# Kernel tuning notes

Measured on AMD Instinct MI355X. Metric: run time of the kernel, lower is better.

## Reference

```python
import jax, jax.numpy as jnp
import numpy as np

D_MODEL = 1024
HEADS = 16
DK = D_MODEL // HEADS
B, S = 2, 2048


def setup_inputs() -> dict:
    key = jax.random.key(0)
    ks = jax.random.split(key, 9)
    s = 0.02
    return {
        "Q": jax.random.normal(ks[0], (B, S, D_MODEL), jnp.float32),
        "K": jax.random.normal(ks[1], (B, S, D_MODEL), jnp.float32),
        "V": jax.random.normal(ks[2], (B, S, D_MODEL), jnp.float32),
        "mask": jnp.ones((B, 1, S), jnp.int32),
        "Wq": jax.random.normal(ks[3], (D_MODEL, D_MODEL), jnp.float32) * s,
        "Wk": jax.random.normal(ks[4], (D_MODEL, D_MODEL), jnp.float32) * s,
        "Wv": jax.random.normal(ks[5], (D_MODEL, D_MODEL), jnp.float32) * s,
        "Wo": jax.random.normal(ks[6], (D_MODEL, D_MODEL), jnp.float32) * s,
        "ln_gamma": jnp.ones((D_MODEL,), jnp.float32),
        "ln_beta": jnp.zeros((D_MODEL,), jnp.float32),
    }


def _layer_norm(x, gamma, beta, eps=1e-5):
    mu = jnp.mean(x, axis=-1, keepdims=True)
    var = jnp.mean(jnp.square(x - mu), axis=-1, keepdims=True)
    return (x - mu) * jax.lax.rsqrt(var + eps) * gamma + beta


def reference(Q, K, V, mask, Wq, Wk, Wv, Wo, ln_gamma, ln_beta):
    # torch Linear(no bias): y = x @ W.T
    def split_heads(x):  # [B,S,D] -> [B,H,S,dk]
        return x.reshape(B, -1, HEADS, DK).transpose(0, 2, 1, 3)

    q = split_heads(Q @ Wq.T)
    k = split_heads(K @ Wk.T)
    v = split_heads(V @ Wv.T)

    # scores: [B,H,Sq,Sk]
    scores = jnp.einsum("bhqd,bhkd->bhqk", q, k) / np.sqrt(DK).astype(np.float32)
    m = mask[:, None, :, :]  # [B,1,1,S] broadcast over heads and queries
    scores = jnp.where(m == 0, -jnp.inf, scores)
    attn = jax.nn.softmax(scores, axis=-1)  # dropout is identity in eval
    out = jnp.einsum("bhqk,bhkd->bhqd", attn, v)
    out = out.transpose(0, 2, 1, 3).reshape(B, -1, D_MODEL)
    out = out @ Wo.T
    return _layer_norm(out + Q, ln_gamma, ln_beta)
```

## Files before the change

kernel.cpp:

```cpp
#include <hip/hip_runtime.h>
#include <hip/hip_bf16.h>
#include <stdint.h>

#define NB 2
#define NS 2048
#define ND 1024
#define NH 16
#define NDK 64
#define NM (NB*NS)

using bf16x8 = __attribute__((ext_vector_type(8))) short;
using f32x4  = __attribute__((ext_vector_type(4))) float;
using f32x16 = __attribute__((ext_vector_type(16))) float;
using u32x4  = __attribute__((ext_vector_type(4))) unsigned;

__device__ __forceinline__ unsigned short f2bf(float f){
  unsigned u = __float_as_uint(f);
  u += 0x7fffu + ((u>>16)&1u);
  return (unsigned short)(u>>16);
}

__device__ __forceinline__ void gload_lds16(const void* g, void* l){
  __builtin_amdgcn_global_load_lds((const __attribute__((address_space(1))) void*)g,
                                   (__attribute__((address_space(3))) void*)l, 16, 0, 0);
}

__device__ __forceinline__ float fexp2(float x){
#if __has_builtin(__builtin_amdgcn_exp2f)
  return __builtin_amdgcn_exp2f(x);
#else
  return __expf(x * 0.69314718056f);
#endif
}

__device__ __forceinline__ unsigned cvtpk_bf16(float lo, float hi){
  unsigned r;
  asm("v_cvt_pk_bf16_f32 %0, %1, %2" : "=v"(r) : "v"(lo), "v"(hi));
  return r;
}

__device__ __forceinline__ void swap32(unsigned &a, unsigned &b){
#if __has_builtin(__builtin_amdgcn_permlane32_swap)
  auto rr = __builtin_amdgcn_permlane32_swap((int)a, (int)b, false, false);
  a = (unsigned)rr[0]; b = (unsigned)rr[1];
#else
  const bool lo = (threadIdx.x & 32) == 0;
  unsigned sa = (unsigned)__shfl_xor((int)a, 32, 64);
  unsigned sb = (unsigned)__shfl_xor((int)b, 32, 64);
  unsigned na = lo ? a : sb;
  unsigned nb = lo ? sa : b;
  a = na; b = nb;
#endif
}

__device__ __forceinline__ f32x16 mfma32(bf16x8 a, bf16x8 b, f32x16 c){
  return __builtin_amdgcn_mfma_f32_32x32x16_bf16(a, b, c, 0, 0, 0);
}

__global__ __launch_bounds__(256) void prep_k(const float* __restrict__ Q, const float* __restrict__ K,
                                              const float* __restrict__ V, const float* __restrict__ Wq,
                                              const float* __restrict__ Wk, const float* __restrict__ Wv,
                                              const float* __restrict__ Wo,
                                              unsigned short* __restrict__ Xbf,
                                              unsigned short* __restrict__ Wbf){
  const int bid = blockIdx.x;
  const float* src; unsigned short* dst; int i;
  if (bid < 12288){
    const int which = bid >> 12;
    src = (which==0) ? Q : (which==1) ? K : V;
    dst = Xbf + ((size_t)which << 22);
    i = (bid & 4095)*256 + threadIdx.x;
  } else {
    const int which = (bid - 12288) >> 10;
    src = (which==0) ? Wq : (which==1) ? Wk : (which==2) ? Wv : Wo;
    dst = Wbf + ((size_t)which << 20);
    i = ((bid - 12288) & 1023)*256 + threadIdx.x;
  }
  float4 v = ((const float4*)src)[i];
  ushort4 o;
  o.x = f2bf(v.x); o.y = f2bf(v.y); o.z = f2bf(v.z); o.w = f2bf(v.w);
  ((ushort4*)dst)[i] = o;
}

__device__ void gemm128_core(const short* __restrict__ A, const short* __restrict__ W,
                             void* __restrict__ out, int mode){
  __shared__ short lsA[2][4096];
  __shared__ short lsB[2][4096];
  const int tid = threadIdx.x;
  const int m0 = blockIdx.y*128, n0 = blockIdx.x*128;
  const short* gA = A + (size_t)m0*1024;
  const short* gB = W + (size_t)n0*1024;
  const int srow = tid>>2, scol = (tid&3)*8;
  const int w = tid>>6, lane = tid&63, lr = lane&15, lk = lane>>4;
  const int wm = w>>1, wn = w&1;

  f32x4 acc[4][4];
  #pragma unroll
  for (int i=0;i<4;++i)
    #pragma unroll
    for (int j=0;j<4;++j) acc[i][j] = (f32x4){0.f,0.f,0.f,0.f};

  #pragma unroll
  for (int r=0;r<2;++r){
    gload_lds16(gA + (size_t)(r*64+srow)*1024 + scol, &lsA[0][(r*256+tid)*8]);
    gload_lds16(gB + (size_t)(r*64+srow)*1024 + scol, &lsB[0][(r*256+tid)*8]);
  }
  int cur = 0;
  for (int ks=0; ks<32; ++ks){
    __syncthreads();
    if (ks+1 < 32){
      const int k0 = (ks+1)*32;
      #pragma unroll
      for (int r=0;r<2;++r){
        gload_lds16(gA + (size_t)(r*64+srow)*1024 + k0 + scol, &lsA[cur^1][(r*256+tid)*8]);
        gload_lds16(gB + (size_t)(r*64+srow)*1024 + k0 + scol, &lsB[cur^1][(r*256+tid)*8]);
      }
    }
    bf16x8 af[4], bfr[4];
    #pragma unroll
    for (int i=0;i<4;++i){
      af[i]  = *(const bf16x8*)&lsA[cur][(wm*64+i*16+lr)*32 + lk*8];
      bfr[i] = *(const bf16x8*)&lsB[cur][(wn*64+i*16+lr)*32 + lk*8];
    }
    #pragma unroll
    for (int i=0;i<4;++i)
      #pragma unroll
      for (int j=0;j<4;++j)
        acc[i][j] = __builtin_amdgcn_mfma_f32_16x16x32_bf16(af[i], bfr[j], acc[i][j], 0,0,0);
    cur ^= 1;
  }
  #pragma unroll
  for (int i=0;i<4;++i)
    #pragma unroll
    for (int j=0;j<4;++j)
      #pragma unroll
      for (int r=0;r<4;++r){
        const int m = m0 + wm*64 + i*16 + lk*4 + r;
        const int n = n0 + wn*64 + j*16 + lr;
        const float v = acc[i][j][r];
        if (mode == 2){
          ((float*)out)[(size_t)m*1024 + n] = v;
        } else {
          const int b = m>>11, s = m&2047, h = n>>6, dk = n&63;
          size_t addr;
          if (mode == 0) addr = (((size_t)(b*NH+h))*NS + s)*NDK + dk;
          else           addr = (((size_t)(b*NH+h))*NDK + dk)*NS + s;
          ((unsigned short*)out)[addr] = f2bf(v);
        }
      }
}

__global__ __launch_bounds__(256) void gemm_qkv(const short* __restrict__ Xbf, const short* __restrict__ Wbf,
                                                unsigned short* qh, unsigned short* kh, unsigned short* vT){
  const int z = blockIdx.z;
  const short* A = Xbf + (size_t)z*NM*ND;
  const short* W = Wbf + (size_t)z*ND*ND;
  void* out = (z==0) ? (void*)qh : (z==1) ? (void*)kh : (void*)vT;
  gemm128_core(A, W, out, (z==2) ? 1 : 0);
}

__global__ __launch_bounds__(256) void gemm_out(const short* __restrict__ Attn, const short* __restrict__ Wo,
                                                float* proj){
  gemm128_core(Attn, Wo, proj, 2);
}

__global__ __launch_bounds__(512) void attn_k(const short* __restrict__ qh, const short* __restrict__ kh,
                                              const short* __restrict__ vT, const int* __restrict__ mask,
                                              unsigned short* __restrict__ attn){
  __shared__ char sb[32768];
  const int bid = blockIdx.x;
  const int qb = bid & 7, h = (bid>>3)&15, b = bid>>7;
  const int tid = threadIdx.x, w = tid>>6, lane = tid&63;
  const int ql = lane & 31, hi = lane>>5;
  const int bh = b*NH + h;
  const int q0 = qb*256 + w*32;
  const float C2 = 0.18033688f;

  const int D = tid*16;
  const int strow = D>>7;
  const int S = D ^ ((strow&7)<<4);
  const char* ksrc  = (const char*)(kh + (size_t)bh*NS*NDK) + S;
  const char* vsrc  = (const char*)(vT + ((size_t)bh*NDK + strow)*NS) + (S & 127);

  const short* qrow = qh + ((size_t)bh*NS + q0 + ql)*NDK + hi*8;
  bf16x8 qf[4];
  #pragma unroll
  for (int kp=0;kp<4;++kp) qf[kp] = *(const bf16x8*)(qrow + kp*16);

  const int* mrow = mask + b*NS;

  f32x16 o0, o1;
  #pragma unroll
  for (int r=0;r<16;++r){ o0[r]=0.f; o1[r]=0.f; }
  float mrun = -1e30f, lrun = 0.f;

  const int swz = (ql&7)<<4;

  gload_lds16(ksrc, sb + D);
  gload_lds16(vsrc, sb + 16384 + D);

  for (int kt=0; kt<32; ++kt){
    const int kv0 = kt*64;
    const int buf = (kt&1)*8192;
    __syncthreads();
    if (kt+1 < 32){
      const int nbuf = ((kt+1)&1)*8192;
      gload_lds16(ksrc + (size_t)(kv0+64)*128, sb + nbuf + D);
      gload_lds16(vsrc + (size_t)(kv0+64)*2,   sb + 16384 + nbuf + D);
    }
    const unsigned long long bal = __ballot(mrow[kv0 + lane] != 0);
    const unsigned mw0 = (unsigned)bal, mw1 = (unsigned)(bal>>32);
    const bool allm = (~bal) == 0ull;

    bf16x8 kf[8];
    #pragma unroll
    for (int kvh=0;kvh<2;++kvh)
      #pragma unroll
      for (int kp=0;kp<4;++kp)
        kf[kvh*4+kp] = *(const bf16x8*)(sb + buf + (((kvh*32+ql)*128 + kp*32 + hi*16) ^ swz));

    f32x16 s0, s1;
    #pragma unroll
    for (int r=0;r<16;++r){ s0[r]=0.f; s1[r]=0.f; }
    #pragma unroll
    for (int kp=0;kp<4;++kp){
      s0 = mfma32(kf[kp],   qf[kp], s0);
      s1 = mfma32(kf[4+kp], qf[kp], s1);
    }

    float t[16];
    #pragma unroll
    for (int r=0;r<16;++r) t[r] = fmaxf(s0[r], s1[r]);
    #pragma unroll
    for (int st=8; st>=1; st>>=1)
      #pragma unroll
      for (int r=0;r<st;++r) t[r] = fmaxf(t[r], t[r+st]);
    const float tm = fmaxf(t[0], __shfl_xor(t[0], 32, 64));

    if (!__all(tm - mrun <= 32.f)){
      const float mnew = fmaxf(mrun, tm);
      const float fac  = fexp2((mrun - mnew)*C2);
      mrun = mnew;
      #pragma unroll
      for (int r=0;r<16;++r){ o0[r]*=fac; o1[r]*=fac; }
      lrun *= fac;
    }
    const float nb = mrun*C2;

    bf16x8 vf[8];
    #pragma unroll
    for (int dh=0;dh<2;++dh)
      #pragma unroll
      for (int c=0;c<4;++c)
        vf[dh*4+c] = *(const bf16x8*)(sb + 16384 + buf + (((dh*32+ql)*128 + c*32 + hi*16) ^ swz));

    float psum = 0.f;
    #pragma unroll
    for (int kvh=0; kvh<2; ++kvh){
      const f32x16& ss = kvh ? s1 : s0;
      const unsigned mw = kvh ? mw1 : mw0;
      unsigned pwd[8];
      float ps0 = 0.f, ps1 = 0.f;
      #pragma unroll
      for (int i=0;i<8;++i){
        const int bp0 = ((2*i)&3) + 8*((2*i)>>2);
        float p0 = fexp2(ss[2*i]*C2   - nb);
        float p1 = fexp2(ss[2*i+1]*C2 - nb);
        if (!allm){
          p0 = ((mw >> (bp0     + 4*hi)) & 1u) ? p0 : 0.f;
          p1 = ((mw >> (bp0 + 1 + 4*hi)) & 1u) ? p1 : 0.f;
        }
        ps0 += p0; ps1 += p1;
        pwd[i] = cvtpk_bf16(p0, p1);
      }
      psum += ps0 + ps1;
      swap32(pwd[0], pwd[2]);
      swap32(pwd[1], pwd[3]);
      swap32(pwd[4], pwd[6]);
      swap32(pwd[5], pwd[7]);
      u32x4 c0w = {pwd[0], pwd[1], pwd[2], pwd[3]};
      u32x4 c1w = {pwd[4], pwd[5], pwd[6], pwd[7]};
      bf16x8 pf0 = __builtin_bit_cast(bf16x8, c0w);
      bf16x8 pf1 = __builtin_bit_cast(bf16x8, c1w);
      o0 = mfma32(vf[0*4 + 2*kvh],     pf0, o0);
      o1 = mfma32(vf[1*4 + 2*kvh],     pf0, o1);
      o0 = mfma32(vf[0*4 + 2*kvh + 1], pf1, o0);
      o1 = mfma32(vf[1*4 + 2*kvh + 1], pf1, o1);
    }
    psum += __shfl_xor(psum, 32, 64);
    lrun += psum;
  }

  __syncthreads();
  const float inv = 1.f / lrun;
  char* ep = sb + w*4096;
  #pragma unroll
  for (int dh=0; dh<2; ++dh){
    const f32x16& oo = dh ? o1 : o0;
    #pragma unroll
    for (int i=0;i<8;++i){
      const int d0 = ((2*i)&3) + 8*((2*i)>>2) + 4*hi + dh*32;
      const unsigned pk = cvtpk_bf16(oo[2*i]*inv, oo[2*i+1]*inv);
      *(unsigned*)(ep + (((ql*128) + d0*2) ^ ((ql&7)<<4))) = pk;
    }
  }
  asm volatile("s_waitcnt lgkmcnt(0)" ::: "memory");
  #pragma unroll
  for (int seg=0; seg<4; ++seg){
    const int qq = seg*8 + (lane>>3), dc = (lane&7)*8;
    bf16x8 vv = *(const bf16x8*)(ep + (((qq*128) + dc*2) ^ ((qq&7)<<4)));
    *(bf16x8*)(attn + ((size_t)b*NS + q0 + qq)*ND + h*NDK + dc) = vv;
  }
}

__global__ __launch_bounds__(256) void ln_k(const float* __restrict__ proj, const float* __restrict__ Qin,
                                            const float* __restrict__ gamma, const float* __restrict__ beta,
                                            float* __restrict__ out){
  const int row = blockIdx.x*4 + (threadIdx.x>>6);
  const int lane = threadIdx.x & 63;
  const float4* pp = (const float4*)(proj + (size_t)row*ND);
  const float4* qq = (const float4*)(Qin + (size_t)row*ND);
  float4 x[4];
  float sum = 0.f;
  #pragma unroll
  for (int i=0;i<4;++i){
    const float4 a = pp[lane + i*64];
    const float4 bq = qq[lane + i*64];
    x[i].x = a.x+bq.x; x[i].y = a.y+bq.y; x[i].z = a.z+bq.z; x[i].w = a.w+bq.w;
    sum += x[i].x + x[i].y + x[i].z + x[i].w;
  }
  #pragma unroll
  for (int off=32; off>=1; off>>=1) sum += __shfl_xor(sum, off, 64);
  const float mu = sum * (1.f/1024.f);
  float vs = 0.f;
  #pragma unroll
  for (int i=0;i<4;++i){
    float d0=x[i].x-mu, d1=x[i].y-mu, d2=x[i].z-mu, d3=x[i].w-mu;
    vs += d0*d0 + d1*d1 + d2*d2 + d3*d3;
  }
  #pragma unroll
  for (int off=32; off>=1; off>>=1) vs += __shfl_xor(vs, off, 64);
  const float rstd = rsqrtf(vs*(1.f/1024.f) + 1e-5f);
  #pragma unroll
  for (int i=0;i<4;++i){
    const float4 g  = ((const float4*)gamma)[lane + i*64];
    const float4 be = ((const float4*)beta)[lane + i*64];
    float4 y;
    y.x = (x[i].x-mu)*rstd*g.x + be.x;
    y.y = (x[i].y-mu)*rstd*g.y + be.y;
    y.z = (x[i].z-mu)*rstd*g.z + be.z;
    y.w = (x[i].w-mu)*rstd*g.w + be.w;
    ((float4*)(out + (size_t)row*ND))[lane + i*64] = y;
  }
}

extern "C" void kernel_launch(void* const* d_in, const int* in_sizes, int n_in,
                              void* d_out, int out_size, void* d_ws, size_t ws_size,
                              hipStream_t stream){
  const float* Q    = (const float*)d_in[0];
  const float* K    = (const float*)d_in[1];
  const float* V    = (const float*)d_in[2];
  const int*   mask = (const int*)  d_in[3];
  const float* Wq   = (const float*)d_in[4];
  const float* Wk   = (const float*)d_in[5];
  const float* Wv   = (const float*)d_in[6];
  const float* Wo   = (const float*)d_in[7];
  const float* gam  = (const float*)d_in[8];
  const float* bet  = (const float*)d_in[9];
  float* out = (float*)d_out;
  char* ws = (char*)d_ws;

  unsigned short* Wbf  = (unsigned short*)(ws);
  unsigned short* Xbf  = (unsigned short*)(ws + (size_t)(8u<<20));
  unsigned short* qhp  = (unsigned short*)(ws + (size_t)(32u<<20));
  unsigned short* khp  = (unsigned short*)(ws + (size_t)(40u<<20));
  unsigned short* vTp  = (unsigned short*)(ws + (size_t)(48u<<20));
  unsigned short* attb = (unsigned short*)(ws + (size_t)(56u<<20));
  float* proj  = (float*)(ws + (size_t)(8u<<20));

  prep_k<<<16384,256,0,stream>>>(Q, K, V, Wq, Wk, Wv, Wo, Xbf, Wbf);

  gemm_qkv<<<dim3(8,32,3),256,0,stream>>>((const short*)Xbf, (const short*)Wbf, qhp, khp, vTp);

  attn_k<<<256,512,0,stream>>>((const short*)qhp, (const short*)khp, (const short*)vTp, mask, attb);

  gemm_out<<<dim3(8,32),256,0,stream>>>((const short*)attb, (const short*)(Wbf + (3u<<20)), proj);

  ln_k<<<1024,256,0,stream>>>(proj, Q, gam, bet, out);
}
```

Baseline: 171.6 us.

## Use 256x128 QKV GEMM tiles, XCD-aware block remap, fuse residual into out-proj

The QKV projection GEMM now computes a 256x128 tile per block, with two A sub-tiles sharing each B fragment, which halves the number of B loads per output. Launches are flattened to 1D and blocks are remapped so neighbouring logical tiles land on the same XCD, which should improve L2 reuse. The residual add of Q moves into the output-projection GEMM epilogue, so the layer-norm kernel no longer reads Q. The trade-off is more accumulator registers (32 f32x4 per thread) and only 384 blocks in the QKV GEMM, which may lower occupancy.

```diff
diff --git a/kernel.cpp b/kernel.cpp
--- a/kernel.cpp
+++ b/kernel.cpp
@@ -82,28 +82,40 @@
   ((ushort4*)dst)[i] = o;
 }
 
-__device__ void gemm128_core(const short* __restrict__ A, const short* __restrict__ W,
-                             void* __restrict__ out, int mode){
-  __shared__ short lsA[2][4096];
+__global__ __launch_bounds__(256) void gemm_qkv(const short* __restrict__ Xbf, const short* __restrict__ Wbf,
+                                                unsigned short* __restrict__ qh, unsigned short* __restrict__ kh,
+                                                unsigned short* __restrict__ vT){
+  __shared__ short lsA[2][2][4096];
   __shared__ short lsB[2][4096];
   const int tid = threadIdx.x;
-  const int m0 = blockIdx.y*128, n0 = blockIdx.x*128;
-  const short* gA = A + (size_t)m0*1024;
-  const short* gB = W + (size_t)n0*1024;
+  const int hw = blockIdx.x;
+  const int logical = (hw & 7)*48 + (hw >> 3);
+  const int z = logical >> 7, rem = logical & 127;
+  const int my = rem >> 3, nx = rem & 7;
+  const short* A = Xbf + (size_t)z*NM*ND;
+  const short* W = Wbf + (size_t)z*ND*ND;
+  unsigned short* out = (z==0) ? qh : (z==1) ? kh : vT;
+  const int mode = (z==2) ? 1 : 0;
+  const int m0 = my*256, n0 = nx*128;
+
+  const short* gA0 = A + (size_t)m0*1024;
+  const short* gA1 = A + (size_t)(m0+128)*1024;
+  const short* gB  = W + (size_t)n0*1024;
   const int srow = tid>>2, scol = (tid&3)*8;
   const int w = tid>>6, lane = tid&63, lr = lane&15, lk = lane>>4;
   const int wm = w>>1, wn = w&1;
 
-  f32x4 acc[4][4];
+  f32x4 acc0[4][4], acc1[4][4];
   #pragma unroll
   for (int i=0;i<4;++i)
     #pragma unroll
-    for (int j=0;j<4;++j) acc[i][j] = (f32x4){0.f,0.f,0.f,0.f};
+    for (int j=0;j<4;++j){ acc0[i][j] = (f32x4){0.f,0.f,0.f,0.f}; acc1[i][j] = (f32x4){0.f,0.f,0.f,0.f}; }
 
   #pragma unroll
   for (int r=0;r<2;++r){
-    gload_lds16(gA + (size_t)(r*64+srow)*1024 + scol, &lsA[0][(r*256+tid)*8]);
-    gload_lds16(gB + (size_t)(r*64+srow)*1024 + scol, &lsB[0][(r*256+tid)*8]);
+    gload_lds16(gA0 + (size_t)(r*64+srow)*1024 + scol, &lsA[0][0][(r*256+tid)*8]);
+    gload_lds16(gA1 + (size_t)(r*64+srow)*1024 + scol, &lsA[0][1][(r*256+tid)*8]);
+    gload_lds16(gB  + (size_t)(r*64+srow)*1024 + scol, &lsB[0][(r*256+tid)*8]);
   }
   int cur = 0;
   for (int ks=0; ks<32; ++ks){
@@ -112,56 +124,111 @@
       const int k0 = (ks+1)*32;
       #pragma unroll
       for (int r=0;r<2;++r){
-        gload_lds16(gA + (size_t)(r*64+srow)*1024 + k0 + scol, &lsA[cur^1][(r*256+tid)*8]);
-        gload_lds16(gB + (size_t)(r*64+srow)*1024 + k0 + scol, &lsB[cur^1][(r*256+tid)*8]);
+        gload_lds16(gA0 + (size_t)(r*64+srow)*1024 + k0 + scol, &lsA[cur^1][0][(r*256+tid)*8]);
+        gload_lds16(gA1 + (size_t)(r*64+srow)*1024 + k0 + scol, &lsA[cur^1][1][(r*256+tid)*8]);
+        gload_lds16(gB  + (size_t)(r*64+srow)*1024 + k0 + scol, &lsB[cur^1][(r*256+tid)*8]);
       }
     }
-    bf16x8 af[4], bfr[4];
-    #pragma unroll
-    for (int i=0;i<4;++i){
-      af[i]  = *(const bf16x8*)&lsA[cur][(wm*64+i*16+lr)*32 + lk*8];
-      bfr[i] = *(const bf16x8*)&lsB[cur][(wn*64+i*16+lr)*32 + lk*8];
-    }
+    bf16x8 bfr[4], af[4];
+    #pragma unroll
+    for (int j=0;j<4;++j) bfr[j] = *(const bf16x8*)&lsB[cur][(wn*64+j*16+lr)*32 + lk*8];
+    #pragma unroll
+    for (int i=0;i<4;++i) af[i] = *(const bf16x8*)&lsA[cur][0][(wm*64+i*16+lr)*32 + lk*8];
     #pragma unroll
     for (int i=0;i<4;++i)
       #pragma unroll
       for (int j=0;j<4;++j)
-        acc[i][j] = __builtin_amdgcn_mfma_f32_16x16x32_bf16(af[i], bfr[j], acc[i][j], 0,0,0);
+        acc0[i][j] = __builtin_amdgcn_mfma_f32_16x16x32_bf16(af[i], bfr[j], acc0[i][j], 0,0,0);
+    #pragma unroll
+    for (int i=0;i<4;++i) af[i] = *(const bf16x8*)&lsA[cur][1][(wm*64+i*16+lr)*32 + lk*8];
+    #pragma unroll
+    for (int i=0;i<4;++i)
+      #pragma unroll
+      for (int j=0;j<4;++j)
+        acc1[i][j] = __builtin_amdgcn_mfma_f32_16x16x32_bf16(af[i], bfr[j], acc1[i][j], 0,0,0);
     cur ^= 1;
   }
   #pragma unroll
-  for (int i=0;i<4;++i)
-    #pragma unroll
-    for (int j=0;j<4;++j)
-      #pragma unroll
-      for (int r=0;r<4;++r){
-        const int m = m0 + wm*64 + i*16 + lk*4 + r;
-        const int n = n0 + wn*64 + j*16 + lr;
-        const float v = acc[i][j][r];
-        if (mode == 2){
-          ((float*)out)[(size_t)m*1024 + n] = v;
-        } else {
+  for (int sub=0; sub<2; ++sub){
+    const int mb = m0 + sub*128;
+    #pragma unroll
+    for (int i=0;i<4;++i)
+      #pragma unroll
+      for (int j=0;j<4;++j)
+        #pragma unroll
+        for (int r=0;r<4;++r){
+          const int m = mb + wm*64 + i*16 + lk*4 + r;
+          const int n = n0 + wn*64 + j*16 + lr;
+          const float v = sub ? acc1[i][j][r] : acc0[i][j][r];
           const int b = m>>11, s = m&2047, h = n>>6, dk = n&63;
           size_t addr;
           if (mode == 0) addr = (((size_t)(b*NH+h))*NS + s)*NDK + dk;
           else           addr = (((size_t)(b*NH+h))*NDK + dk)*NS + s;
-          ((unsigned short*)out)[addr] = f2bf(v);
+          out[addr] = f2bf(v);
         }
+  }
+}
+
+__global__ __launch_bounds__(256) void gemm_out(const short* __restrict__ Attn, const short* __restrict__ Wo,
+                                                const float* __restrict__ Qin, float* __restrict__ proj){
+  __shared__ short lsA[2][4096];
+  __shared__ short lsB[2][4096];
+  const int tid = threadIdx.x;
+  const int hw = blockIdx.x;
+  const int logical = (hw & 7)*32 + (hw >> 3);
+  const int my = logical >> 3, nx = logical & 7;
+  const int m0 = my*128, n0 = nx*128;
+  const short* gA = Attn + (size_t)m0*1024;
+  const short* gB = Wo + (size_t)n0*1024;
+  const int srow = tid>>2, scol = (tid&3)*8;
+  const int w = tid>>6, lane = tid&63, lr = lane&15, lk = lane>>4;
+  const int wm = w>>1, wn = w&1;
+
+  f32x4 acc[4][4];
+  #pragma unroll
+  for (int i=0;i<4;++i)
+    #pragma unroll
+    for (int j=0;j<4;++j) acc[i][j] = (f32x4){0.f,0.f,0.f,0.f};
+
+  #pragma unroll
+  for (int r=0;r<2;++r){
+    gload_lds16(gA + (size_t)(r*64+srow)*1024 + scol, &lsA[0][(r*256+tid)*8]);
+    gload_lds16(gB + (size_t)(r*64+srow)*1024 + scol, &lsB[0][(r*256+tid)*8]);
+  }
+  int cur = 0;
+  for (int ks=0; ks<32; ++ks){
+    __syncthreads();
+    if (ks+1 < 32){
+      const int k0 = (ks+1)*32;
+      #pragma unroll
+      for (int r=0;r<2;++r){
+        gload_lds16(gA + (size_t)(r*64+srow)*1024 + k0 + scol, &lsA[cur^1][(r*256+tid)*8]);
+        gload_lds16(gB + (size_t)(r*64+srow)*1024 + k0 + scol, &lsB[cur^1][(r*256+tid)*8]);
       }
-}
-
-__global__ __launch_bounds__(256) void gemm_qkv(const short* __restrict__ Xbf, const short* __restrict__ Wbf,
-                                                unsigned short* qh, unsigned short* kh, unsigned short* vT){
-  const int z = blockIdx.z;
-  const short* A = Xbf + (size_t)z*NM*ND;
-  const short* W = Wbf + (size_t)z*ND*ND;
-  void* out = (z==0) ? (void*)qh : (z==1) ? (void*)kh : (void*)vT;
-  gemm128_core(A, W, out, (z==2) ? 1 : 0);
-}
-
-__global__ __launch_bounds__(256) void gemm_out(const short* __restrict__ Attn, const short* __restrict__ Wo,
-                                                float* proj){
-  gemm128_core(Attn, Wo, proj, 2);
+    }
+    bf16x8 af[4], bfr[4];
+    #pragma unroll
+    for (int i=0;i<4;++i){
+      af[i]  = *(const bf16x8*)&lsA[cur][(wm*64+i*16+lr)*32 + lk*8];
+      bfr[i] = *(const bf16x8*)&lsB[cur][(wn*64+i*16+lr)*32 + lk*8];
+    }
+    #pragma unroll
+    for (int i=0;i<4;++i)
+      #pragma unroll
+      for (int j=0;j<4;++j)
+        acc[i][j] = __builtin_amdgcn_mfma_f32_16x16x32_bf16(af[i], bfr[j], acc[i][j], 0,0,0);
+    cur ^= 1;
+  }
+  #pragma unroll
+  for (int i=0;i<4;++i)
+    #pragma unroll
+    for (int j=0;j<4;++j)
+      #pragma unroll
+      for (int r=0;r<4;++r){
+        const int m = m0 + wm*64 + i*16 + lk*4 + r;
+        const int n = n0 + wn*64 + j*16 + lr;
+        proj[(size_t)m*1024 + n] = acc[i][j][r] + Qin[(size_t)m*1024 + n];
+      }
 }
 
 __global__ __launch_bounds__(512) void attn_k(const short* __restrict__ qh, const short* __restrict__ kh,
@@ -313,20 +380,17 @@
   }
 }
 
-__global__ __launch_bounds__(256) void ln_k(const float* __restrict__ proj, const float* __restrict__ Qin,
+__global__ __launch_bounds__(256) void ln_k(const float* __restrict__ proj,
                                             const float* __restrict__ gamma, const float* __restrict__ beta,
                                             float* __restrict__ out){
   const int row = blockIdx.x*4 + (threadIdx.x>>6);
   const int lane = threadIdx.x & 63;
   const float4* pp = (const float4*)(proj + (size_t)row*ND);
-  const float4* qq = (const float4*)(Qin + (size_t)row*ND);
   float4 x[4];
   float sum = 0.f;
   #pragma unroll
   for (int i=0;i<4;++i){
-    const float4 a = pp[lane + i*64];
-    const float4 bq = qq[lane + i*64];
-    x[i].x = a.x+bq.x; x[i].y = a.y+bq.y; x[i].z = a.z+bq.z; x[i].w = a.w+bq.w;
+    x[i] = pp[lane + i*64];
     sum += x[i].x + x[i].y + x[i].z + x[i].w;
   }
   #pragma unroll
@@ -380,11 +444,11 @@
 
   prep_k<<<16384,256,0,stream>>>(Q, K, V, Wq, Wk, Wv, Wo, Xbf, Wbf);
 
-  gemm_qkv<<<dim3(8,32,3),256,0,stream>>>((const short*)Xbf, (const short*)Wbf, qhp, khp, vTp);
+  gemm_qkv<<<384,256,0,stream>>>((const short*)Xbf, (const short*)Wbf, qhp, khp, vTp);
 
   attn_k<<<256,512,0,stream>>>((const short*)qhp, (const short*)khp, (const short*)vTp, mask, attb);
 
-  gemm_out<<<dim3(8,32),256,0,stream>>>((const short*)attb, (const short*)(Wbf + (3u<<20)), proj);
-
-  ln_k<<<1024,256,0,stream>>>(proj, Q, gam, bet, out);
-}
+  gemm_out<<<256,256,0,stream>>>((const short*)attb, (const short*)(Wbf + (3u<<20)), Q, proj);
+
+  ln_k<<<1024,256,0,stream>>>(proj, gam, bet, out);
+}
```

Result: slower. 179.5 us (+4.6%).
